# Kernel tuning notes

Measured on AMD Instinct MI355X. Metric: run time of the kernel, lower is better.

## Reference

```python
import jax, jax.numpy as jnp
import numpy as np

B, CIN, CNECK, COUT = 8, 128, 128, 256
NV, NF = 10242, 20480  # icosphere level 5: nv = 10*4^5+2, nf = 20*4^5
EPS = 1e-5


def spmatmul(x, rows, cols, vals, m):
    # x: [..., N]; out[..., r] += vals[k] * x[..., cols[k]] for rows[k] == r
    g = x[..., cols] * vals
    return jnp.zeros(x.shape[:-1] + (m,), x.dtype).at[..., rows].add(g)


def conv1x1(x, w, b):
    # x: [B, Cin, N], w: [Cout, Cin], b: [Cout]
    return jnp.einsum('oi,bin->bon', w, x) + b[None, :, None]


def batchnorm1d(x, gamma, beta):
    # training-mode BN over (batch, spatial) per channel, biased variance
    mean = jnp.mean(x, axis=(0, 2), keepdims=True)
    var = jnp.var(x, axis=(0, 2), keepdims=True)
    xhat = (x - mean) * jax.lax.rsqrt(var + EPS)
    return gamma[None, :, None] * xhat + beta[None, :, None]


def setup_inputs() -> dict:
    key = jax.random.key(0)
    ks = jax.random.split(key, 16)

    def coo(k, nrows, per_row, ncols, scale):
        rows = jnp.repeat(jnp.arange(nrows, dtype=jnp.int32), per_row)
        cols = jax.random.randint(k, (nrows * per_row,), 0, ncols, dtype=jnp.int32)
        vals = jax.random.normal(jax.random.fold_in(k, 1), (nrows * per_row,), jnp.float32) * scale
        return rows, cols, vals

    Gr, Gc, Gv = coo(ks[0], 3 * NF, 3, NV, 0.5)
    Lr, Lc, Lv = coo(ks[1], NV, 7, NV, 0.3)
    Fr, Fc, Fv = coo(ks[2], NV, 6, NF, 1.0 / 6.0)

    def nrm(k, shape, scale=1.0):
        return jax.random.normal(k, shape, jnp.float32) * scale

    s_in = 1.0 / np.sqrt(CIN)
    s_nk = 1.0 / np.sqrt(CNECK)
    s_cf = 1.0 / np.sqrt(4 * CNECK)
    return {
        'x': nrm(ks[3], (B, CIN, NV)),
        'w1a': nrm(ks[4], (CNECK, CIN), s_in), 'b1a': nrm(ks[5], (CNECK,), s_in),
        'g1a': jnp.ones((CNECK,), jnp.float32), 'be1a': jnp.zeros((CNECK,), jnp.float32),
        'coeffs': nrm(ks[6], (CNECK * 4, CNECK), s_cf),
        'g2a': jnp.ones((CNECK,), jnp.float32), 'be2a': jnp.zeros((CNECK,), jnp.float32),
        'w3a': nrm(ks[7], (COUT, CNECK), s_nk), 'b3a': nrm(ks[8], (COUT,), s_nk),
        'g3a': jnp.ones((COUT,), jnp.float32), 'be3a': jnp.zeros((COUT,), jnp.float32),
        'w1b': nrm(ks[9], (COUT, CIN), s_in), 'b1b': nrm(ks[10], (COUT,), s_in),
        'g1b': jnp.ones((COUT,), jnp.float32), 'be1b': jnp.zeros((COUT,), jnp.float32),
        'G_vals': Gv, 'L_vals': Lv, 'F2V_vals': Fv,
        'EW': nrm(ks[11], (NF, 3)), 'NS': nrm(ks[12], (NF, 3)),
        'G_rows': Gr, 'G_cols': Gc,
        'L_rows': Lr, 'L_cols': Lc,
        'F2V_rows': Fr, 'F2V_cols': Fc,
    }


def mesh_conv(h, coeffs, G_rows, G_cols, G_vals, L_rows, L_cols, L_vals,
              F2V_rows, F2V_cols, F2V_vals, EW, NS):
    b, c, nv = h.shape
    # gradient on faces: [B,C,3*NF] -> [B,C,3,NF] -> [B,C,NF,3]
    grad_face = spmatmul(h, G_rows, G_cols, G_vals, 3 * NF)
    grad_face = grad_face.reshape(b, c, 3, NF).transpose(0, 1, 3, 2)
    laplacian = spmatmul(h, L_rows, L_cols, L_vals, NV)
    identity = h  # stride=1 => nv_prev == nv
    gf_ew = jnp.sum(grad_face * EW, axis=-1)  # [B,C,NF]
    gf_ns = jnp.sum(grad_face * NS, axis=-1)
    gv_ew = spmatmul(gf_ew, F2V_rows, F2V_cols, F2V_vals, NV)
    gv_ns = spmatmul(gf_ns, F2V_rows, F2V_cols, F2V_vals, NV)
    feat = jnp.stack([identity, laplacian, gv_ew, gv_ns], axis=-1)  # [B,C,NV,4]
    # [B,NV,C*4] @ [C*4,Cout] -> [B,Cout,NV]  (note: no bias added in original forward)
    out = jnp.matmul(feat.transpose(0, 2, 1, 3).reshape(b, nv, c * 4), coeffs)
    return out.transpose(0, 2, 1)


def reference(x, w1a, b1a, g1a, be1a, coeffs, g2a, be2a, w3a, b3a, g3a, be3a,
              w1b, b1b, g1b, be1b, G_vals, L_vals, F2V_vals, EW, NS,
              G_rows, G_cols, L_rows, L_cols, F2V_rows, F2V_cols):
    # shortcut branch: conv_1b -> bn_1b
    x2 = batchnorm1d(conv1x1(x, w1b, b1b), g1b, be1b)
    # main branch
    h = jax.nn.relu(batchnorm1d(conv1x1(x, w1a, b1a), g1a, be1a))
    h = mesh_conv(h, coeffs, G_rows, G_cols, G_vals, L_rows, L_cols, L_vals,
                  F2V_rows, F2V_cols, F2V_vals, EW, NS)
    h = jax.nn.relu(batchnorm1d(h, g2a, be2a))
    x1 = batchnorm1d(conv1x1(h, w3a, b3a), g3a, be3a)
    return jax.nn.relu(x1 + x2)
```

## Files before the change

kernel.cpp:

```cpp
#include <hip/hip_runtime.h>
#include <math.h>

#define BB   8
#define NVV  10242
#define NFF  20480
#define EPSBN 1e-5f
#define GRAM_BLOCKS 644

typedef __attribute__((ext_vector_type(8))) short bf16x8_t;
typedef __attribute__((ext_vector_type(4))) float f32x4_t;

__device__ inline float bf2f(ushort u) {
    union { uint i; float f; } v; v.i = ((uint)u) << 16; return v.f;
}
__device__ inline ushort f2bf(float f) {
    union { float f; uint i; } v; v.f = f;
    const uint r = v.i + 0x7fffu + ((v.i >> 16) & 1u);
    return (ushort)(r >> 16);
}
__device__ inline void unpack2(uint w, float& lo, float& hi) {
    union { uint i; float f; } a, b;
    a.i = w << 16; b.i = w & 0xffff0000u;
    lo = a.f; hi = b.f;
}
__device__ inline uint pack2(float lo, float hi) {
    return (uint)f2bf(lo) | ((uint)f2bf(hi) << 16);
}
__device__ inline void fma8(const uint4 hv, const float w, float s[8]) {
    float lo, hi;
    unpack2(hv.x, lo, hi); s[0] = fmaf(w, lo, s[0]); s[1] = fmaf(w, hi, s[1]);
    unpack2(hv.y, lo, hi); s[2] = fmaf(w, lo, s[2]); s[3] = fmaf(w, hi, s[3]);
    unpack2(hv.z, lo, hi); s[4] = fmaf(w, lo, s[4]); s[5] = fmaf(w, hi, s[5]);
    unpack2(hv.w, lo, hi); s[6] = fmaf(w, lo, s[6]); s[7] = fmaf(w, hi, s[7]);
}
__device__ inline uint4 pack8(const float s[8]) {
    uint4 p;
    p.x = pack2(s[0], s[1]); p.y = pack2(s[2], s[3]);
    p.z = pack2(s[4], s[5]); p.w = pack2(s[6], s[7]);
    return p;
}

__global__ __launch_bounds__(256)
void gram_kernel(const float* __restrict__ x, float* __restrict__ gramPart,
                 float* __restrict__ xsumPart, uint* __restrict__ xTu)
{
    __shared__ __align__(16) ushort Ahi[128 * 64];
    __shared__ __align__(16) ushort Alo[128 * 64];
    const int t = threadIdx.x;
    const int l = t & 63, wid = t >> 6;
    const int l15 = l & 15, l4 = l >> 4;
    f32x4_t acc[2][8];
#pragma unroll
    for (int m = 0; m < 2; ++m)
#pragma unroll
        for (int n = 0; n < 8; ++n) acc[m][n] = (f32x4_t){0.f, 0.f, 0.f, 0.f};
    float xs[8] = {0.f, 0.f, 0.f, 0.f, 0.f, 0.f, 0.f, 0.f};

    for (int s = 0; s < 2; ++s) {
        const int cc = blockIdx.x * 2 + s;
        const int b = cc / 161, tb = cc % 161, v0 = tb * 64;
#pragma unroll
        for (int i = 0; i < 8; ++i) {
            const int item = t + (i << 8);
            const int c = item >> 4, vq = item & 15;
            const int gv = v0 + (vq << 2);
            const float* xp = x + ((size_t)b * 128 + c) * NVV + gv;
            float4 xv = make_float4(0.f, 0.f, 0.f, 0.f);
            if (gv + 4 <= NVV) {
                xv = *reinterpret_cast<const float4*>(xp);
            } else {
                if (gv     < NVV) xv.x = xp[0];
                if (gv + 1 < NVV) xv.y = xp[1];
            }
            xs[i] += xv.x + xv.y + xv.z + xv.w;
            const ushort h0 = f2bf(xv.x), h1 = f2bf(xv.y), h2 = f2bf(xv.z), h3 = f2bf(xv.w);
            const ushort e0 = f2bf(xv.x - bf2f(h0)), e1 = f2bf(xv.y - bf2f(h1));
            const ushort e2 = f2bf(xv.z - bf2f(h2)), e3 = f2bf(xv.w - bf2f(h3));
            uint2 hp, lp;
            hp.x = (uint)h0 | ((uint)h1 << 16); hp.y = (uint)h2 | ((uint)h3 << 16);
            lp.x = (uint)e0 | ((uint)e1 << 16); lp.y = (uint)e2 | ((uint)e3 << 16);
            const int byte = (c << 7) + (vq << 3);
            const int swz = byte ^ ((c & 7) << 4);
            *reinterpret_cast<uint2*>((char*)Ahi + swz) = hp;
            *reinterpret_cast<uint2*>((char*)Alo + swz) = lp;
        }
        __syncthreads();
        {
            const int v = t & 63, cq = t >> 6;
            const int gv = v0 + v;
            if (gv < NVV) {
                uint4* rowp = reinterpret_cast<uint4*>(xTu + ((size_t)b * NVV + gv) * 64) + (cq << 2);
#pragma unroll
                for (int k2 = 0; k2 < 4; ++k2) {
                    uint wrd[4];
#pragma unroll
                    for (int w2 = 0; w2 < 4; ++w2) {
                        const int c0 = (cq << 5) + (k2 << 3) + (w2 << 1);
                        const int b0 = ((c0) << 7) + (v << 1);
                        const int b1 = ((c0 + 1) << 7) + (v << 1);
                        const ushort q0 = *reinterpret_cast<const ushort*>((const char*)Ahi + (b0 ^ ((c0 & 7) << 4)));
                        const ushort q1 = *reinterpret_cast<const ushort*>((const char*)Ahi + (b1 ^ (((c0 + 1) & 7) << 4)));
                        wrd[w2] = (uint)q0 | ((uint)q1 << 16);
                    }
                    rowp[k2] = make_uint4(wrd[0], wrd[1], wrd[2], wrd[3]);
                }
            }
        }
#pragma unroll
        for (int kk2 = 0; kk2 < 2; ++kk2) {
            bf16x8_t ah[2], al[2];
#pragma unroll
            for (int m = 0; m < 2; ++m) {
                const int row = wid * 32 + m * 16 + l15;
                const int byte = (row << 7) + (kk2 << 6) + (l4 << 4);
                ah[m] = *reinterpret_cast<const bf16x8_t*>((const char*)Ahi + (byte ^ ((row & 7) << 4)));
                al[m] = *reinterpret_cast<const bf16x8_t*>((const char*)Alo + (byte ^ ((row & 7) << 4)));
            }
#pragma unroll
            for (int n = 0; n < 8; ++n) {
                const int rn = n * 16 + l15;
                const int byte = (rn << 7) + (kk2 << 6) + (l4 << 4);
                const bf16x8_t bh = *reinterpret_cast<const bf16x8_t*>((const char*)Ahi + (byte ^ ((rn & 7) << 4)));
                const bf16x8_t bl = *reinterpret_cast<const bf16x8_t*>((const char*)Alo + (byte ^ ((rn & 7) << 4)));
#pragma unroll
                for (int m = 0; m < 2; ++m) {
                    acc[m][n] = __builtin_amdgcn_mfma_f32_16x16x32_bf16(ah[m], bh, acc[m][n], 0, 0, 0);
                    acc[m][n] = __builtin_amdgcn_mfma_f32_16x16x32_bf16(ah[m], bl, acc[m][n], 0, 0, 0);
                    acc[m][n] = __builtin_amdgcn_mfma_f32_16x16x32_bf16(al[m], bh, acc[m][n], 0, 0, 0);
                }
            }
        }
        __syncthreads();
    }
    float* gp = gramPart + (size_t)blockIdx.x * 16384;
#pragma unroll
    for (int m = 0; m < 2; ++m)
#pragma unroll
        for (int n = 0; n < 8; ++n)
#pragma unroll
            for (int j = 0; j < 4; ++j) {
                const int row = wid * 32 + m * 16 + l4 * 4 + j;
                const int col = n * 16 + l15;
                gp[row * 128 + col] = acc[m][n][j];
            }
#pragma unroll
    for (int i = 0; i < 8; ++i) {
        xs[i] += __shfl_xor(xs[i], 1);
        xs[i] += __shfl_xor(xs[i], 2);
        xs[i] += __shfl_xor(xs[i], 4);
        xs[i] += __shfl_xor(xs[i], 8);
    }
    if ((l & 15) == 0) {
#pragma unroll
        for (int i = 0; i < 8; ++i)
            xsumPart[(size_t)blockIdx.x * 128 + wid * 4 + l4 + i * 16] = xs[i];
    }
}

__global__ void reduce_gram_kernel(const float* __restrict__ gp, const float* __restrict__ xp,
                                   float* __restrict__ Gram, float* __restrict__ xsum)
{
    const int tid = blockIdx.x * 256 + threadIdx.x;
    for (int e = tid; e < 16384; e += 64 * 256) {
        float s = 0.f;
        for (int i = 0; i < GRAM_BLOCKS; ++i) s += gp[(size_t)i * 16384 + e];
        Gram[e] = s;
    }
    if (blockIdx.x == 0 && threadIdx.x < 128) {
        float s = 0.f;
        for (int i = 0; i < GRAM_BLOCKS; ++i) s += xp[(size_t)i * 128 + threadIdx.x];
        xsum[threadIdx.x] = s;
    }
}

__global__ __launch_bounds__(128)
void stats_ab_kernel(const float* __restrict__ Gram, const float* __restrict__ xsum,
                     const float* __restrict__ w1a, const float* __restrict__ g1a,
                     const float* __restrict__ be1a,
                     const float* __restrict__ w1b, const float* __restrict__ g1b,
                     const float* __restrict__ be1b,
                     float* __restrict__ alpha_a, float* __restrict__ beta_a,
                     float* __restrict__ alpha_b, float* __restrict__ beta_b)
{
    const int t = threadIdx.x;
    const int cc = blockIdx.x;
    const float invN = 1.f / (float)(BB * NVV);
    const bool isA = cc < 128;
    const int c = isA ? cc : cc - 128;
    const float* Wrow = isA ? (w1a + (size_t)c * 128) : (w1b + (size_t)c * 128);
    __shared__ float Wr[128];
    __shared__ float red[4];
    Wr[t] = Wrow[t];
    __syncthreads();
    float gi = 0.f;
    const float* Grow = Gram + (size_t)t * 128;
    for (int j = 0; j < 128; ++j) gi = fmaf(Grow[j], Wr[j], gi);
    float pi = Wr[t] * gi * invN;
    float qi = (xsum[t] * invN) * Wr[t];
    for (int off = 32; off > 0; off >>= 1) {
        pi += __shfl_down(pi, off);
        qi += __shfl_down(qi, off);
    }
    const int wid = t >> 6;
    if ((t & 63) == 0) { red[wid] = pi; red[2 + wid] = qi; }
    __syncthreads();
    if (t == 0) {
        const float P = red[0] + red[1], Q = red[2] + red[3];
        const float var = P - Q * Q;
        const float g = isA ? g1a[c] : g1b[c];
        const float be = isA ? be1a[c] : be1b[c];
        const float a = g * rsqrtf(var + EPSBN);
        if (isA) { alpha_a[c] = a; beta_a[c] = be - a * Q; }
        else     { alpha_b[c] = a; beta_b[c] = be - a * Q; }
    }
}

__global__ __launch_bounds__(256)
void prepack_weights_kernel(const float* __restrict__ w1a, const float* __restrict__ w1b,
                            const float* __restrict__ w3a, uint* __restrict__ wpk)
{
    const int j = blockIdx.x * 256 + threadIdx.x;
    const int seg = j >> 12;
    const int slab = seg >> 1, kc = (seg & 1) << 6;
    const int u = j & 4095;
    const int o = u >> 5;
    const int inner = (u << 2) & 127;
    const int inner0 = inner ^ ((o & 7) << 4);
    const int kp = inner0 >> 2;
    const float* W;
    if (slab == 0)      W = w1a;
    else if (slab <= 2) W = w1b + (size_t)(slab - 1) * 128 * 128;
    else                W = w3a + (size_t)(slab - 3) * 128 * 128;
    const float2 wv = *reinterpret_cast<const float2*>(&W[(size_t)o * 128 + kc + 2 * kp]);
    wpk[j] = pack2(wv.x, wv.y);
}

__global__ __launch_bounds__(256)
void prepack_coeffs_kernel(const float* __restrict__ coeffs, uint* __restrict__ cpk)
{
    const int j = blockIdx.x * 256 + threadIdx.x;
    const int chunk = j >> 12, u = j & 4095;
    const int o = u >> 5;
    const int inner = (u << 2) & 127;
    const int inner0 = inner ^ ((o & 7) << 4);
    const int p = inner0 >> 2;
    const int q = chunk >> 1, c0 = (chunk & 1) << 6;
    const int row0 = (c0 + 2 * p) * 4 + q;
    cpk[j] = pack2(coeffs[(size_t)row0 * 128 + o], coeffs[(size_t)(row0 + 4) * 128 + o]);
}

template <int MODE>
__global__ __launch_bounds__(256)
void mfma_conv_kernel(const ushort* __restrict__ Asrc, const uint4* __restrict__ wpk,
                      const float* __restrict__ aIn, const float* __restrict__ bIn,
                      const float* __restrict__ aA, const float* __restrict__ bA,
                      const float* __restrict__ aB, const float* __restrict__ bB,
                      ushort* __restrict__ hOut, ushort* __restrict__ x2Out,
                      ushort* __restrict__ x1Out,
                      float* __restrict__ statSum, float* __restrict__ statSsq)
{
    __shared__ __align__(16) ushort As[64 * 128];
    __shared__ __align__(16) ushort Bs[128 * 64];
    __shared__ float statS[512], statQ[512];
    const int t = threadIdx.x;
    const int bid = blockIdx.x;
    const int b = bid & 7, vblk = bid >> 3;
    const int v0 = vblk * 64;
    const int l = t & 63, wid = t >> 6;
    const int l15 = l & 15, l4 = l >> 4;

#pragma unroll
    for (int i = 0; i < 4; ++i) {
        const int item = t + (i << 8);
        const int r = item >> 4, piece = item & 15;
        const int cb = piece * 8;
        const int v = v0 + r;
        uint4 pk = make_uint4(0u, 0u, 0u, 0u);
        if (v < NVV) {
            pk = *reinterpret_cast<const uint4*>(Asrc + ((size_t)b * NVV + v) * 128 + cb);
            if (MODE == 1) {
                float s[8];
                unpack2(pk.x, s[0], s[1]); unpack2(pk.y, s[2], s[3]);
                unpack2(pk.z, s[4], s[5]); unpack2(pk.w, s[6], s[7]);
                const float4 a0 = *reinterpret_cast<const float4*>(&aIn[cb]);
                const float4 a1 = *reinterpret_cast<const float4*>(&aIn[cb + 4]);
                const float4 b0 = *reinterpret_cast<const float4*>(&bIn[cb]);
                const float4 b1 = *reinterpret_cast<const float4*>(&bIn[cb + 4]);
                s[0] = fmaxf(fmaf(a0.x, s[0], b0.x), 0.f);
                s[1] = fmaxf(fmaf(a0.y, s[1], b0.y), 0.f);
                s[2] = fmaxf(fmaf(a0.z, s[2], b0.z), 0.f);
                s[3] = fmaxf(fmaf(a0.w, s[3], b0.w), 0.f);
                s[4] = fmaxf(fmaf(a1.x, s[4], b1.x), 0.f);
                s[5] = fmaxf(fmaf(a1.y, s[5], b1.y), 0.f);
                s[6] = fmaxf(fmaf(a1.z, s[6], b1.z), 0.f);
                s[7] = fmaxf(fmaf(a1.w, s[7], b1.w), 0.f);
                pk = pack8(s);
            }
        }
        const int byte = (r << 8) + (piece << 4);
        *reinterpret_cast<uint4*>((char*)As + (byte ^ ((r & 7) << 4))) = pk;
    }

    const int NZ = (MODE == 0) ? 3 : 2;
    for (int z = 0; z < NZ; ++z) {
        const int slab = (MODE == 0) ? z : (3 + z);
        f32x4_t acc[8];
#pragma unroll
        for (int n = 0; n < 8; ++n) acc[n] = (f32x4_t){0.f, 0.f, 0.f, 0.f};

        for (int kc = 0; kc < 128; kc += 64) {
            const uint4* wseg = wpk + (size_t)(slab * 2 + (kc >> 6)) * 1024;
#pragma unroll
            for (int i = 0; i < 4; ++i)
                reinterpret_cast<uint4*>(Bs)[t + (i << 8)] = wseg[t + (i << 8)];
            __syncthreads();
#pragma unroll
            for (int kk2 = 0; kk2 < 2; ++kk2) {
                const int row = wid * 16 + l15;
                const int abyte = (row << 8) + (kc << 1) + (kk2 << 6) + (l4 << 4);
                const bf16x8_t af = *reinterpret_cast<const bf16x8_t*>(
                    (const char*)As + (abyte ^ ((row & 7) << 4)));
#pragma unroll
                for (int n = 0; n < 8; ++n) {
                    const int o = n * 16 + l15;
                    const int bbyte = (o << 7) + (kk2 << 6) + (l4 << 4);
                    const bf16x8_t bfr = *reinterpret_cast<const bf16x8_t*>(
                        (const char*)Bs + (bbyte ^ ((o & 7) << 4)));
                    acc[n] = __builtin_amdgcn_mfma_f32_16x16x32_bf16(af, bfr, acc[n], 0, 0, 0);
                }
            }
            __syncthreads();
        }

        if (MODE == 0 && z == 0) {
            float aO[8], bO[8];
#pragma unroll
            for (int n = 0; n < 8; ++n) {
                const int c = n * 16 + l15;
                aO[n] = aA[c]; bO[n] = bA[c];
            }
#pragma unroll
            for (int j = 0; j < 4; ++j) {
                const int v = v0 + wid * 16 + l4 * 4 + j;
                if (v < NVV) {
                    ushort* mp = hOut + ((size_t)b * NVV + v) * 128 + l15;
#pragma unroll
                    for (int n = 0; n < 8; ++n)
                        mp[n * 16] = f2bf(fmaxf(fmaf(aO[n], acc[n][j], bO[n]), 0.f));
                }
            }
        } else if (MODE == 0) {
            float aO[8], bO[8];
#pragma unroll
            for (int n = 0; n < 8; ++n) {
                const int cl = n * 16 + l15;
                aO[n] = aB[(z - 1) * 128 + cl]; bO[n] = bB[(z - 1) * 128 + cl];
            }
            const int vbase = v0 + wid * 16 + l4 * 4;
#pragma unroll
            for (int n = 0; n < 8; ++n) {
                const int cl = n * 16 + l15;
                const int ch = (z - 1) * 128 + cl;
                ushort* p = x2Out + ((size_t)b * 256 + ch) * NVV + vbase;
                if (vbase + 4 <= NVV) {
                    uint* pu = (uint*)p;
                    pu[0] = pack2(fmaf(aO[n], acc[n][0], bO[n]),
                                  fmaf(aO[n], acc[n][1], bO[n]));
                    pu[1] = pack2(fmaf(aO[n], acc[n][2], bO[n]),
                                  fmaf(aO[n], acc[n][3], bO[n]));
                } else {
#pragma unroll
                    for (int j = 0; j < 4; ++j)
                        if (vbase + j < NVV)
                            p[j] = f2bf(fmaf(aO[n], acc[n][j], bO[n]));
                }
            }
        } else {
            float ss[8], sq[8];
#pragma unroll
            for (int n = 0; n < 8; ++n) { ss[n] = 0.f; sq[n] = 0.f; }
            const int vbase = v0 + wid * 16 + l4 * 4;
#pragma unroll
            for (int n = 0; n < 8; ++n) {
                const int cl = n * 16 + l15;
                const int ch = z * 128 + cl;
                ushort* p = x1Out + ((size_t)b * 256 + ch) * NVV + vbase;
                if (vbase + 4 <= NVV) {
                    float v0f = acc[n][0], v1f = acc[n][1];
                    float v2f = acc[n][2], v3f = acc[n][3];
                    uint* pu = (uint*)p;
                    pu[0] = pack2(v0f, v1f);
                    pu[1] = pack2(v2f, v3f);
                    ss[n] += v0f + v1f + v2f + v3f;
                    sq[n] = fmaf(v0f, v0f, sq[n]); sq[n] = fmaf(v1f, v1f, sq[n]);
                    sq[n] = fmaf(v2f, v2f, sq[n]); sq[n] = fmaf(v3f, v3f, sq[n]);
                } else {
#pragma unroll
                    for (int j = 0; j < 4; ++j) {
                        if (vbase + j < NVV) {
                            const float val = acc[n][j];
                            p[j] = f2bf(val);
                            ss[n] += val;
                            sq[n] = fmaf(val, val, sq[n]);
                        }
                    }
                }
            }
#pragma unroll
            for (int n = 0; n < 8; ++n) {
                ss[n] += __shfl_xor(ss[n], 16); ss[n] += __shfl_xor(ss[n], 32);
                sq[n] += __shfl_xor(sq[n], 16); sq[n] += __shfl_xor(sq[n], 32);
            }
            if (l < 16) {
#pragma unroll
                for (int n = 0; n < 8; ++n) {
                    statS[wid * 128 + n * 16 + l] = ss[n];
                    statQ[wid * 128 + n * 16 + l] = sq[n];
                }
            }
            __syncthreads();
            if (t < 128) {
                const int slot = b * 161 + vblk;
                statSum[((size_t)z * 1288 + slot) * 128 + t] =
                    statS[t] + statS[128 + t] + statS[256 + t] + statS[384 + t];
                statSsq[((size_t)z * 1288 + slot) * 128 + t] =
                    statQ[t] + statQ[128 + t] + statQ[256 + t] + statQ[384 + t];
            }
            __syncthreads();
        }
    }
}

__global__ __launch_bounds__(256)
void face_kernel(const ushort* __restrict__ h, const float* __restrict__ Gv,
                 const int* __restrict__ Gc, const float* __restrict__ EW,
                 const float* __restrict__ NSm, ushort* __restrict__ gf)
{
    const int t = threadIdx.x;
    const int lane = t & 63, wid = t >> 6;
    const int bid = blockIdx.x;
    const int b = bid & 7;
    const int f = (bid >> 3) * 4 + wid;
    const uint* hb = (const uint*)h + (size_t)b * NVV * 64;
    float ewx = 0.f, ewy = 0.f, nsx = 0.f, nsy = 0.f;
#pragma unroll
    for (int e = 0; e < 3; ++e) {
        const size_t r3 = ((size_t)e * NFF + f) * 3;
        float gx = 0.f, gy = 0.f;
#pragma unroll
        for (int j = 0; j < 3; ++j) {
            const float w = Gv[r3 + j];
            const int col = Gc[r3 + j];
            const uint hv = hb[(size_t)col * 64 + lane];
            float lo, hi; unpack2(hv, lo, hi);
            gx = fmaf(w, lo, gx); gy = fmaf(w, hi, gy);
        }
        const float we = EW[f * 3 + e], wn = NSm[f * 3 + e];
        ewx = fmaf(we, gx, ewx); ewy = fmaf(we, gy, ewy);
        nsx = fmaf(wn, gx, nsx); nsy = fmaf(wn, gy, nsy);
    }
    uint* go = (uint*)gf + ((size_t)b * NFF + f) * 128;
    go[lane]      = pack2(ewx, ewy);
    go[64 + lane] = pack2(nsx, nsy);
}

__global__ __launch_bounds__(256)
void mesh_gemm_kernel(const ushort* __restrict__ h, const ushort* __restrict__ gf,
                      const uint4* __restrict__ cpk,
                      const float* __restrict__ Lv, const int* __restrict__ Lc,
                      const float* __restrict__ Fv, const int* __restrict__ Fc,
                      ushort* __restrict__ meshraw,
                      float* __restrict__ msum, float* __restrict__ mssq)
{
    __shared__ __align__(16) ushort As[64 * 64];
    __shared__ __align__(16) ushort Bs[128 * 64];
    __shared__ float statS[512], statQ[512];
    __shared__ int   LciS[448];
    __shared__ float LwS[448];
    __shared__ int   FciS[384];
    __shared__ float FwS[384];
    const int t = threadIdx.x;
    const int bid = blockIdx.x;
    const int b = bid & 7;
    const int vblk = bid >> 3;
    const int v0 = vblk * 64;
    const int l = t & 63, wid = t >> 6;
    const int l15 = l & 15, l4 = l >> 4;
    const size_t hb = (size_t)b * NVV * 128;

    for (int i = t; i < 448; i += 256) {
        const int g = v0 * 7 + i;
        if (g < NVV * 7) { LciS[i] = Lc[g]; LwS[i] = Lv[g]; }
    }
    for (int i = t; i < 384; i += 256) {
        const int g = v0 * 6 + i;
        if (g < NVV * 6) { FciS[i] = Fc[g]; FwS[i] = Fv[g]; }
    }
    __syncthreads();

    f32x4_t acc[8];
#pragma unroll
    for (int n = 0; n < 8; ++n) acc[n] = (f32x4_t){0.f, 0.f, 0.f, 0.f};

    for (int chunk = 0; chunk < 8; ++chunk) {
        const int q = chunk >> 1, c0 = (chunk & 1) << 6;
#pragma unroll
        for (int i = 0; i < 2; ++i) {
            const int item = t + (i << 8);
            const int r = item >> 3, piece = item & 7;
            const int cb = c0 + piece * 8;
            const int v = v0 + r;
            uint4 pk = make_uint4(0u, 0u, 0u, 0u);
            if (v < NVV) {
                if (q == 0) {
                    pk = *reinterpret_cast<const uint4*>(h + hb + (size_t)v * 128 + cb);
                } else if (q == 1) {
                    float s[8] = {0.f, 0.f, 0.f, 0.f, 0.f, 0.f, 0.f, 0.f};
#pragma unroll
                    for (int j = 0; j < 7; ++j) {
                        const float w = LwS[r * 7 + j];
                        const int col = LciS[r * 7 + j];
                        const uint4 hv = *reinterpret_cast<const uint4*>(h + hb + (size_t)col * 128 + cb);
                        fma8(hv, w, s);
                    }
                    pk = pack8(s);
                } else {
                    const int slab = q - 2;
                    float s[8] = {0.f, 0.f, 0.f, 0.f, 0.f, 0.f, 0.f, 0.f};
#pragma unroll
                    for (int j = 0; j < 6; ++j) {
                        const float w = FwS[r * 6 + j];
                        const int f = FciS[r * 6 + j];
                        const uint4 gv = *reinterpret_cast<const uint4*>(
                            gf + (((size_t)b * NFF + f) * 2 + slab) * 128 + cb);
                        fma8(gv, w, s);
                    }
                    pk = pack8(s);
                }
            }
            const int byte = (r << 7) + (piece << 4);
            *reinterpret_cast<uint4*>((char*)As + (byte ^ ((r & 7) << 4))) = pk;
        }
#pragma unroll
        for (int i = 0; i < 4; ++i) {
            const int idx = t + (i << 8);
            reinterpret_cast<uint4*>(Bs)[idx] = cpk[chunk * 1024 + idx];
        }
        __syncthreads();
#pragma unroll
        for (int kk2 = 0; kk2 < 2; ++kk2) {
            const int row = wid * 16 + l15;
            const int abyte = (row << 7) + (kk2 << 6) + (l4 << 4);
            const bf16x8_t af = *reinterpret_cast<const bf16x8_t*>(
                (const char*)As + (abyte ^ ((row & 7) << 4)));
#pragma unroll
            for (int n = 0; n < 8; ++n) {
                const int o = n * 16 + l15;
                const int bbyte = (o << 7) + (kk2 << 6) + (l4 << 4);
                const bf16x8_t bfr = *reinterpret_cast<const bf16x8_t*>(
                    (const char*)Bs + (bbyte ^ ((o & 7) << 4)));
                acc[n] = __builtin_amdgcn_mfma_f32_16x16x32_bf16(af, bfr, acc[n], 0, 0, 0);
            }
        }
        __syncthreads();
    }
    float ss[8], sq[8];
#pragma unroll
    for (int n = 0; n < 8; ++n) { ss[n] = 0.f; sq[n] = 0.f; }
#pragma unroll
    for (int j = 0; j < 4; ++j) {
        const int row = wid * 16 + l4 * 4 + j;
        const int v = v0 + row;
        if (v < NVV) {
            ushort* mp = meshraw + hb + (size_t)v * 128 + l15;
#pragma unroll
            for (int n = 0; n < 8; ++n) {
                const float val = acc[n][j];
                mp[n * 16] = f2bf(val);
                ss[n] += val;
                sq[n] = fmaf(val, val, sq[n]);
            }
        }
    }
#pragma unroll
    for (int n = 0; n < 8; ++n) {
        ss[n] += __shfl_xor(ss[n], 16); ss[n] += __shfl_xor(ss[n], 32);
        sq[n] += __shfl_xor(sq[n], 16); sq[n] += __shfl_xor(sq[n], 32);
    }
    if (l < 16) {
#pragma unroll
        for (int n = 0; n < 8; ++n) {
            statS[wid * 128 + n * 16 + l] = ss[n];
            statQ[wid * 128 + n * 16 + l] = sq[n];
        }
    }
    __syncthreads();
    if (t < 128) {
        const int blk = b * 161 + vblk;
        msum[(size_t)blk * 128 + t] = statS[t] + statS[128 + t] + statS[256 + t] + statS[384 + t];
        mssq[(size_t)blk * 128 + t] = statQ[t] + statQ[128 + t] + statQ[256 + t] + statQ[384 + t];
    }
}

__global__ __launch_bounds__(256)
void finalize_stats_kernel(const float* __restrict__ s, const float* __restrict__ q, int count,
                           const float* __restrict__ g, const float* __restrict__ be,
                           float* __restrict__ alpha, float* __restrict__ beta, int split)
{
    const int c = blockIdx.x, t = threadIdx.x;
    const size_t base = split ? ((size_t)(c >> 7) * count * 128 + (c & 127)) : (size_t)c;
    float ls = 0.f, lq = 0.f;
    for (int i = t; i < count; i += 256) {
        ls += s[base + (size_t)i * 128];
        lq += q[base + (size_t)i * 128];
    }
    __shared__ float rs[256], rq[256];
    rs[t] = ls; rq[t] = lq;
    __syncthreads();
    for (int off = 128; off > 0; off >>= 1) {
        if (t < off) { rs[t] += rs[t + off]; rq[t] += rq[t + off]; }
        __syncthreads();
    }
    if (t == 0) {
        const float invN = 1.f / (float)(BB * NVV);
        const float mean = rs[0] * invN;
        const float var = rq[0] * invN - mean * mean;
        const float a = g[c] * rsqrtf(var + EPSBN);
        alpha[c] = a;
        beta[c] = be[c] - a * mean;
    }
}

__global__ __launch_bounds__(256)
void final_kernel(float* __restrict__ out, const ushort* __restrict__ x1,
                  const ushort* __restrict__ x2,
                  const float* __restrict__ alpha3, const float* __restrict__ beta3)
{
    const int blk = blockIdx.x;
    const int o = blk & 255;
    const float a = alpha3[o], bb = beta3[o];
    float2* po = reinterpret_cast<float2*>(out + (size_t)blk * NVV);
    const uint* p1 = reinterpret_cast<const uint*>(x1 + (size_t)blk * NVV);
    const uint* p2 = reinterpret_cast<const uint*>(x2 + (size_t)blk * NVV);
    for (int i = threadIdx.x; i < NVV / 2; i += 256) {
        float a1, b1, a2, b2;
        unpack2(p1[i], a1, b1);
        unpack2(p2[i], a2, b2);
        po[i] = make_float2(fmaxf(fmaf(a, a1, bb) + a2, 0.f),
                            fmaxf(fmaf(a, b1, bb) + b2, 0.f));
    }
}

extern "C" void kernel_launch(void* const* d_in, const int* in_sizes, int n_in,
                              void* d_out, int out_size, void* d_ws, size_t ws_size,
                              hipStream_t stream)
{
    (void)in_sizes; (void)n_in; (void)out_size;
    const float* x      = (const float*)d_in[0];
    const float* w1a    = (const float*)d_in[1];
    const float* g1a    = (const float*)d_in[3];
    const float* be1a   = (const float*)d_in[4];
    const float* coeffs = (const float*)d_in[5];
    const float* g2a    = (const float*)d_in[6];
    const float* be2a   = (const float*)d_in[7];
    const float* w3a    = (const float*)d_in[8];
    const float* g3a    = (const float*)d_in[10];
    const float* be3a   = (const float*)d_in[11];
    const float* w1b    = (const float*)d_in[12];
    const float* g1b    = (const float*)d_in[14];
    const float* be1b   = (const float*)d_in[15];
    const float* Gv     = (const float*)d_in[16];
    const float* Lv     = (const float*)d_in[17];
    const float* Fv     = (const float*)d_in[18];
    const float* EW     = (const float*)d_in[19];
    const float* NSm    = (const float*)d_in[20];
    const int*   Gc     = (const int*)d_in[22];
    const int*   Lc     = (const int*)d_in[24];
    const int*   Fc     = (const int*)d_in[26];

    char* base = (char*)d_ws;
    size_t off = 0;
    auto alloc = [&](size_t bytes) { char* p = base + off; off += (bytes + 255) & ~(size_t)255; return p; };

    const size_t gfBytes = (size_t)BB * NFF * 2 * 128 * 2;
    char* region0   = alloc(gfBytes);
    float* gramPart = (float*)region0;
    float* xsumPart = (float*)(region0 + (size_t)GRAM_BLOCKS * 16384 * 4);
    ushort* gf      = (ushort*)region0;
    ushort* x1      = (ushort*)region0;

    ushort* xT      = (ushort*)alloc((size_t)BB * NVV * 128 * 2);
    ushort* h       = (ushort*)alloc((size_t)BB * NVV * 128 * 2);
    ushort* meshraw = (ushort*)alloc((size_t)BB * NVV * 128 * 2);
    ushort* x2      = (ushort*)alloc((size_t)BB * 256 * NVV * 2);
    uint*  cpk      = (uint*)alloc(32768 * 4);
    uint*  wpk      = (uint*)alloc(40960 * 4);
    float* Gram     = (float*)alloc(16384 * 4);
    float* xsum     = (float*)alloc(128 * 4);
    float* alpha_a  = (float*)alloc(128 * 4);
    float* beta_a   = (float*)alloc(128 * 4);
    float* alpha_b  = (float*)alloc(256 * 4);
    float* beta_b   = (float*)alloc(256 * 4);
    float* alpha2   = (float*)alloc(128 * 4);
    float* beta2    = (float*)alloc(128 * 4);
    float* alpha3   = (float*)alloc(256 * 4);
    float* beta3    = (float*)alloc(256 * 4);
    float* msum     = (float*)alloc((size_t)1288 * 128 * 4);
    float* mssq     = (float*)alloc((size_t)1288 * 128 * 4);
    float* x1sum    = (float*)alloc((size_t)2 * 1288 * 128 * 4);
    float* x1ssq    = (float*)alloc((size_t)2 * 1288 * 128 * 4);
    if (off > ws_size) return;

    gram_kernel<<<GRAM_BLOCKS, 256, 0, stream>>>(x, gramPart, xsumPart, (uint*)xT);
    reduce_gram_kernel<<<64, 256, 0, stream>>>(gramPart, xsumPart, Gram, xsum);
    stats_ab_kernel<<<384, 128, 0, stream>>>(Gram, xsum, w1a, g1a, be1a, w1b, g1b, be1b,
                                             alpha_a, beta_a, alpha_b, beta_b);
    prepack_coeffs_kernel<<<128, 256, 0, stream>>>(coeffs, cpk);
    prepack_weights_kernel<<<160, 256, 0, stream>>>(w1a, w1b, w3a, wpk);
    mfma_conv_kernel<0><<<1288, 256, 0, stream>>>(
        xT, (const uint4*)wpk, nullptr, nullptr, alpha_a, beta_a, alpha_b, beta_b,
        h, x2, nullptr, nullptr, nullptr);
    face_kernel<<<(NFF / 4) * 8, 256, 0, stream>>>(h, Gv, Gc, EW, NSm, gf);
    mesh_gemm_kernel<<<1288, 256, 0, stream>>>(h, gf, (const uint4*)cpk,
                                               Lv, Lc, Fv, Fc, meshraw, msum, mssq);
    finalize_stats_kernel<<<128, 256, 0, stream>>>(msum, mssq, 1288, g2a, be2a, alpha2, beta2, 0);
    mfma_conv_kernel<1><<<1288, 256, 0, stream>>>(
        meshraw, (const uint4*)wpk, alpha2, beta2, nullptr, nullptr, nullptr, nullptr,
        nullptr, nullptr, x1, x1sum, x1ssq);
    finalize_stats_kernel<<<256, 256, 0, stream>>>(x1sum, x1ssq, 1288, g3a, be3a, alpha3, beta3, 1);
    final_kernel<<<2048, 256, 0, stream>>>((float*)d_out, x1, x2, alpha3, beta3);
}
```

Measured before the change: 301.5 us.

## Read bf16 weight fragments directly from global memory instead of LDS staging

The weight and coefficient prepack kernels now write plain row-major bf16 arrays instead of swizzled packed layouts. The conv and mesh GEMM kernels drop the shared-memory B tile and its per-chunk barriers, loading MFMA B fragments straight from global memory (expected to hit L1/L2 since the weights are small and shared by all blocks). This frees LDS and removes synchronisation, but each wave now issues redundant global loads for the same weight data.

```diff
diff --git a/kernel.cpp b/kernel.cpp
--- a/kernel.cpp
+++ b/kernel.cpp
@@ -217,41 +217,32 @@
 
 __global__ __launch_bounds__(256)
 void prepack_weights_kernel(const float* __restrict__ w1a, const float* __restrict__ w1b,
-                            const float* __restrict__ w3a, uint* __restrict__ wpk)
+                            const float* __restrict__ w3a, ushort* __restrict__ wpku)
 {
     const int j = blockIdx.x * 256 + threadIdx.x;
-    const int seg = j >> 12;
-    const int slab = seg >> 1, kc = (seg & 1) << 6;
-    const int u = j & 4095;
-    const int o = u >> 5;
-    const int inner = (u << 2) & 127;
-    const int inner0 = inner ^ ((o & 7) << 4);
-    const int kp = inner0 >> 2;
+    if (j >= 5 * 16384) return;
+    const int slab = j >> 14, rem = j & 16383;
     const float* W;
     if (slab == 0)      W = w1a;
     else if (slab <= 2) W = w1b + (size_t)(slab - 1) * 128 * 128;
     else                W = w3a + (size_t)(slab - 3) * 128 * 128;
-    const float2 wv = *reinterpret_cast<const float2*>(&W[(size_t)o * 128 + kc + 2 * kp]);
-    wpk[j] = pack2(wv.x, wv.y);
+    wpku[j] = f2bf(W[rem]);
 }
 
 __global__ __launch_bounds__(256)
-void prepack_coeffs_kernel(const float* __restrict__ coeffs, uint* __restrict__ cpk)
+void prepack_coeffs_kernel(const float* __restrict__ coeffs, ushort* __restrict__ cpku)
 {
     const int j = blockIdx.x * 256 + threadIdx.x;
-    const int chunk = j >> 12, u = j & 4095;
-    const int o = u >> 5;
-    const int inner = (u << 2) & 127;
-    const int inner0 = inner ^ ((o & 7) << 4);
-    const int p = inner0 >> 2;
-    const int q = chunk >> 1, c0 = (chunk & 1) << 6;
-    const int row0 = (c0 + 2 * p) * 4 + q;
-    cpk[j] = pack2(coeffs[(size_t)row0 * 128 + o], coeffs[(size_t)(row0 + 4) * 128 + o]);
+    const int chunk = j >> 13, rem = j & 8191;
+    const int o = rem >> 6, k = rem & 63;
+    const int q = chunk >> 1, ch = chunk & 1;
+    const int row = (ch * 64 + k) * 4 + q;
+    cpku[j] = f2bf(coeffs[(size_t)row * 128 + o]);
 }
 
 template <int MODE>
 __global__ __launch_bounds__(256)
-void mfma_conv_kernel(const ushort* __restrict__ Asrc, const uint4* __restrict__ wpk,
+void mfma_conv_kernel(const ushort* __restrict__ Asrc, const ushort* __restrict__ wpku,
                       const float* __restrict__ aIn, const float* __restrict__ bIn,
                       const float* __restrict__ aA, const float* __restrict__ bA,
                       const float* __restrict__ aB, const float* __restrict__ bB,
@@ -260,7 +251,6 @@
                       float* __restrict__ statSum, float* __restrict__ statSsq)
 {
     __shared__ __align__(16) ushort As[64 * 128];
-    __shared__ __align__(16) ushort Bs[128 * 64];
     __shared__ float statS[512], statQ[512];
     const int t = threadIdx.x;
     const int bid = blockIdx.x;
@@ -300,36 +290,29 @@
         const int byte = (r << 8) + (piece << 4);
         *reinterpret_cast<uint4*>((char*)As + (byte ^ ((r & 7) << 4))) = pk;
     }
+    __syncthreads();
 
     const int NZ = (MODE == 0) ? 3 : 2;
     for (int z = 0; z < NZ; ++z) {
         const int slab = (MODE == 0) ? z : (3 + z);
+        const ushort* W = wpku + (size_t)slab * 16384;
         f32x4_t acc[8];
 #pragma unroll
         for (int n = 0; n < 8; ++n) acc[n] = (f32x4_t){0.f, 0.f, 0.f, 0.f};
 
-        for (int kc = 0; kc < 128; kc += 64) {
-            const uint4* wseg = wpk + (size_t)(slab * 2 + (kc >> 6)) * 1024;
-#pragma unroll
-            for (int i = 0; i < 4; ++i)
-                reinterpret_cast<uint4*>(Bs)[t + (i << 8)] = wseg[t + (i << 8)];
-            __syncthreads();
-#pragma unroll
-            for (int kk2 = 0; kk2 < 2; ++kk2) {
-                const int row = wid * 16 + l15;
-                const int abyte = (row << 8) + (kc << 1) + (kk2 << 6) + (l4 << 4);
-                const bf16x8_t af = *reinterpret_cast<const bf16x8_t*>(
-                    (const char*)As + (abyte ^ ((row & 7) << 4)));
-#pragma unroll
-                for (int n = 0; n < 8; ++n) {
-                    const int o = n * 16 + l15;
-                    const int bbyte = (o << 7) + (kk2 << 6) + (l4 << 4);
-                    const bf16x8_t bfr = *reinterpret_cast<const bf16x8_t*>(
-                        (const char*)Bs + (bbyte ^ ((o & 7) << 4)));
-                    acc[n] = __builtin_amdgcn_mfma_f32_16x16x32_bf16(af, bfr, acc[n], 0, 0, 0);
-                }
-            }
-            __syncthreads();
+#pragma unroll
+        for (int kq = 0; kq < 4; ++kq) {
+            const int ko = kq * 32 + l4 * 8;
+            const int row = wid * 16 + l15;
+            const int abyte = (row << 8) + ((kq >> 1) << 7) + ((kq & 1) << 6) + (l4 << 4);
+            const bf16x8_t af = *reinterpret_cast<const bf16x8_t*>(
+                (const char*)As + (abyte ^ ((row & 7) << 4)));
+#pragma unroll
+            for (int n = 0; n < 8; ++n) {
+                const int o = n * 16 + l15;
+                const bf16x8_t bfr = *reinterpret_cast<const bf16x8_t*>(W + (size_t)o * 128 + ko);
+                acc[n] = __builtin_amdgcn_mfma_f32_16x16x32_bf16(af, bfr, acc[n], 0, 0, 0);
+            }
         }
 
         if (MODE == 0 && z == 0) {
@@ -466,14 +449,13 @@
 
 __global__ __launch_bounds__(256)
 void mesh_gemm_kernel(const ushort* __restrict__ h, const ushort* __restrict__ gf,
-                      const uint4* __restrict__ cpk,
+                      const ushort* __restrict__ cpku,
                       const float* __restrict__ Lv, const int* __restrict__ Lc,
                       const float* __restrict__ Fv, const int* __restrict__ Fc,
                       ushort* __restrict__ meshraw,
                       float* __restrict__ msum, float* __restrict__ mssq)
 {
     __shared__ __align__(16) ushort As[64 * 64];
-    __shared__ __align__(16) ushort Bs[128 * 64];
     __shared__ float statS[512], statQ[512];
     __shared__ int   LciS[448];
     __shared__ float LwS[448];
@@ -541,24 +523,19 @@
             const int byte = (r << 7) + (piece << 4);
             *reinterpret_cast<uint4*>((char*)As + (byte ^ ((r & 7) << 4))) = pk;
         }
-#pragma unroll
-        for (int i = 0; i < 4; ++i) {
-            const int idx = t + (i << 8);
-            reinterpret_cast<uint4*>(Bs)[idx] = cpk[chunk * 1024 + idx];
-        }
         __syncthreads();
+        const ushort* Cb = cpku + chunk * 8192;
 #pragma unroll
         for (int kk2 = 0; kk2 < 2; ++kk2) {
             const int row = wid * 16 + l15;
             const int abyte = (row << 7) + (kk2 << 6) + (l4 << 4);
             const bf16x8_t af = *reinterpret_cast<const bf16x8_t*>(
                 (const char*)As + (abyte ^ ((row & 7) << 4)));
+            const int kof = kk2 * 32 + l4 * 8;
 #pragma unroll
             for (int n = 0; n < 8; ++n) {
                 const int o = n * 16 + l15;
-                const int bbyte = (o << 7) + (kk2 << 6) + (l4 << 4);
-                const bf16x8_t bfr = *reinterpret_cast<const bf16x8_t*>(
-                    (const char*)Bs + (bbyte ^ ((o & 7) << 4)));
+                const bf16x8_t bfr = *reinterpret_cast<const bf16x8_t*>(Cb + o * 64 + kof);
                 acc[n] = __builtin_amdgcn_mfma_f32_16x16x32_bf16(af, bfr, acc[n], 0, 0, 0);
             }
         }
@@ -693,8 +670,8 @@
     ushort* h       = (ushort*)alloc((size_t)BB * NVV * 128 * 2);
     ushort* meshraw = (ushort*)alloc((size_t)BB * NVV * 128 * 2);
     ushort* x2      = (ushort*)alloc((size_t)BB * 256 * NVV * 2);
-    uint*  cpk      = (uint*)alloc(32768 * 4);
-    uint*  wpk      = (uint*)alloc(40960 * 4);
+    ushort* cpku    = (ushort*)alloc(65536 * 2);
+    ushort* wpku    = (ushort*)alloc(81920 * 2);
     float* Gram     = (float*)alloc(16384 * 4);
     float* xsum     = (float*)alloc(128 * 4);
     float* alpha_a  = (float*)alloc(128 * 4);
@@ -715,17 +692,17 @@
     reduce_gram_kernel<<<64, 256, 0, stream>>>(gramPart, xsumPart, Gram, xsum);
     stats_ab_kernel<<<384, 128, 0, stream>>>(Gram, xsum, w1a, g1a, be1a, w1b, g1b, be1b,
                                              alpha_a, beta_a, alpha_b, beta_b);
-    prepack_coeffs_kernel<<<128, 256, 0, stream>>>(coeffs, cpk);
-    prepack_weights_kernel<<<160, 256, 0, stream>>>(w1a, w1b, w3a, wpk);
+    prepack_coeffs_kernel<<<256, 256, 0, stream>>>(coeffs, cpku);
+    prepack_weights_kernel<<<320, 256, 0, stream>>>(w1a, w1b, w3a, wpku);
     mfma_conv_kernel<0><<<1288, 256, 0, stream>>>(
-        xT, (const uint4*)wpk, nullptr, nullptr, alpha_a, beta_a, alpha_b, beta_b,
+        xT, wpku, nullptr, nullptr, alpha_a, beta_a, alpha_b, beta_b,
         h, x2, nullptr, nullptr, nullptr);
     face_kernel<<<(NFF / 4) * 8, 256, 0, stream>>>(h, Gv, Gc, EW, NSm, gf);
-    mesh_gemm_kernel<<<1288, 256, 0, stream>>>(h, gf, (const uint4*)cpk,
+    mesh_gemm_kernel<<<1288, 256, 0, stream>>>(h, gf, cpku,
                                                Lv, Lc, Fv, Fc, meshraw, msum, mssq);
     finalize_stats_kernel<<<128, 256, 0, stream>>>(msum, mssq, 1288, g2a, be2a, alpha2, beta2, 0);
     mfma_conv_kernel<1><<<1288, 256, 0, stream>>>(
-        meshraw, (const uint4*)wpk, alpha2, beta2, nullptr, nullptr, nullptr, nullptr,
+        meshraw, wpku, alpha2, beta2, nullptr, nullptr, nullptr, nullptr,
         nullptr, nullptr, x1, x1sum, x1ssq);
     finalize_stats_kernel<<<256, 256, 0, stream>>>(x1sum, x1ssq, 1288, g3a, be3a, alpha3, beta3, 1);
     final_kernel<<<2048, 256, 0, stream>>>((float*)d_out, x1, x2, alpha3, beta3);
```

New measurement: 437.5 us. 45.1% more time.
